# Optimization experiments

Measured on AMD Instinct MI355X. Metric: run time of the kernel, lower is better.

Reference implementation:

```python
import jax, jax.numpy as jnp
import numpy as np

T, N = 12, 1000          # frames, pedestrians
RNN, EMB, GS, OUT = 128, 64, 4, 5
G = GS * GS              # 16 grid cells


def lstm_cell(x, h, c, W_ih, W_hh, b_ih, b_hh):
    # PyTorch LSTMCell gate order: i, f, g, o
    gates = x @ W_ih.T + h @ W_hh.T + b_ih + b_hh
    i, f, g, o = jnp.split(gates, 4, axis=-1)
    c_new = jax.nn.sigmoid(f) * c + jax.nn.sigmoid(i) * jnp.tanh(g)
    h_new = jax.nn.sigmoid(o) * jnp.tanh(c_new)
    return h_new, c_new


def setup_inputs() -> dict:
    key = jax.random.key(0)
    ks = jax.random.split(key, 10)
    s = 0.02  # small init scale for weights
    # binary occupancy grid masks: grid[f, n, p, g] = 1 if ped p falls in cell g of ped n's neighborhood
    grids = (jax.random.uniform(ks[1], (T, N, N, G)) < 0.02).astype(jnp.float32)
    return {
        "input_data": jax.random.normal(ks[0], (T, N, 2), dtype=jnp.float32),
        "grids": grids,
        "hidden_states": jnp.zeros((N, RNN), dtype=jnp.float32),
        "cell_states": jnp.zeros((N, RNN), dtype=jnp.float32),
        "W_in": jax.random.normal(ks[2], (EMB, 2)) * s,
        "b_in": jnp.zeros((EMB,), dtype=jnp.float32),
        "W_soc": jax.random.normal(ks[3], (EMB, G * RNN)) * s,
        "b_soc": jnp.zeros((EMB,), dtype=jnp.float32),
        "W_ih": jax.random.normal(ks[4], (4 * RNN, 2 * EMB)) * s,
        "W_hh": jax.random.normal(ks[5], (4 * RNN, RNN)) * s,
        "b_ih": jnp.zeros((4 * RNN,), dtype=jnp.float32),
        "b_hh": jnp.zeros((4 * RNN,), dtype=jnp.float32),
        "W_out": jax.random.normal(ks[6], (OUT, RNN)) * s,
        "b_out": jnp.zeros((OUT,), dtype=jnp.float32),
    }


def reference(input_data, grids, hidden_states, cell_states,
              W_in, b_in, W_soc, b_soc, W_ih, W_hh, b_ih, b_hh, W_out, b_out):
    def step(carry, frame):
        h, c = carry
        x, grid = frame  # x: [N,2], grid: [N,N,G]
        # social pooling: for each node n, grid[n].T @ h  -> [G, RNN]
        social = jnp.einsum('npg,ph->ngh', grid, h).reshape(N, G * RNN)
        ie = jax.nn.relu(x @ W_in.T + b_in)           # [N, EMB]
        te = jax.nn.relu(social @ W_soc.T + b_soc)    # [N, EMB]
        emb = jnp.concatenate([ie, te], axis=-1)      # [N, 2*EMB]
        h, c = lstm_cell(emb, h, c, W_ih, W_hh, b_ih, b_hh)
        out = h @ W_out.T + b_out                     # [N, OUT]
        return (h, c), out

    (h, c), outputs = jax.lax.scan(step, (hidden_states, cell_states),
                                   (input_data, grids))
    return outputs, h, c  # outputs: [T, N, OUT]
```

## Files before the change

kernel.cpp:

```cpp
#include <hip/hip_runtime.h>
#include <hip/hip_bf16.h>


#define TT   12
#define NN   1000
#define RNNW 128
#define EMBW 64
#define GGW  16
#define OUTD 5
#define UCW  (GGW*EMBW)
#define AKW  256
#define NGATE 512
#define GROW (NN*GGW)

__device__ __forceinline__ float sigmf(float x) { return 1.f / (1.f + __expf(-x)); }

__global__ void k_prep(const float* __restrict__ h0, const float* __restrict__ c0,
                       const float* __restrict__ W_soc,
                       const float* __restrict__ W_ih, const float* __restrict__ W_hh,
                       float* __restrict__ h, float* __restrict__ c,
                       float* __restrict__ WsT, float* __restrict__ WcT) {
    int i = blockIdx.x * 256 + threadIdx.x;
    if (i < 131072) {
        int e = i >> 11, gk = i & 2047;
        WsT[gk * 64 + e] = W_soc[i];
    } else if (i < 196608) {
        int i2 = i - 131072;
        int j = i2 >> 7, k = i2 & 127;
        WcT[k * 512 + j] = W_ih[i2];
    } else if (i < 262144) {
        int i3 = i - 196608;
        int j = i3 >> 7, k = i3 & 127;
        WcT[(128 + k) * 512 + j] = W_hh[i3];
    } else if (i < 262144 + NN * RNNW) {
        int i4 = i - 262144; h[i4] = h0[i4];
    } else if (i < 262144 + 2 * NN * RNNW) {
        int i5 = i - 262144 - NN * RNNW; c[i5] = c0[i5];
    }
}

__global__ __launch_bounds__(256) void k_U(const float* __restrict__ h,
                                           const float* __restrict__ WsT,
                                           float* __restrict__ U) {
    __shared__ float sAT[RNNW][64];
    __shared__ float sBT[RNNW][64];
    const int tid = threadIdx.x;
    const int p0 = blockIdx.x * 64;
    const int g  = blockIdx.y;
    {
        int pp = tid >> 2, kq = (tid & 3) * 4;
        int p = p0 + pp;
        #pragma unroll
        for (int pass = 0; pass < 8; ++pass) {
            int k0 = pass * 16 + kq;
            float4 v = {0.f, 0.f, 0.f, 0.f};
            if (p < NN) v = *(const float4*)(h + (size_t)p * RNNW + k0);
            sAT[k0 + 0][pp] = v.x; sAT[k0 + 1][pp] = v.y;
            sAT[k0 + 2][pp] = v.z; sAT[k0 + 3][pp] = v.w;
        }
    }
    {
        #pragma unroll
        for (int pass = 0; pass < 8; ++pass) {
            int f = pass * 256 + tid;
            int k = f >> 4, e4 = (f & 15) * 4;
            float4 v = *(const float4*)(WsT + (size_t)(g * 128 + k) * 64 + e4);
            *(float4*)(&sBT[k][e4]) = v;
        }
    }
    __syncthreads();
    const int tx = tid & 15, ty = tid >> 4;
    float acc[4][4];
    #pragma unroll
    for (int i = 0; i < 4; i++)
        #pragma unroll
        for (int j = 0; j < 4; j++) acc[i][j] = 0.f;
    #pragma unroll 4
    for (int k = 0; k < RNNW; ++k) {
        float4 a4 = *(const float4*)(&sAT[k][ty * 4]);
        float4 b4 = *(const float4*)(&sBT[k][tx * 4]);
        const float av[4] = {a4.x, a4.y, a4.z, a4.w};
        const float bv[4] = {b4.x, b4.y, b4.z, b4.w};
        #pragma unroll
        for (int i = 0; i < 4; i++)
            #pragma unroll
            for (int j = 0; j < 4; j++) acc[i][j] += av[i] * bv[j];
    }
    #pragma unroll
    for (int i = 0; i < 4; i++) {
        int p = p0 + ty * 4 + i;
        if (p < NN) {
            float4 v = {acc[i][0], acc[i][1], acc[i][2], acc[i][3]};
            *(float4*)(U + (size_t)p * UCW + g * EMBW + tx * 4) = v;
        }
    }
}

__global__ __launch_bounds__(512) void k_pool(const unsigned int* __restrict__ grids,
                                              const float* __restrict__ x_in,
                                              const float* __restrict__ U,
                                              const float* __restrict__ h,
                                              const float* __restrict__ W_in,
                                              const float* __restrict__ b_in,
                                              const float* __restrict__ b_soc,
                                              float* __restrict__ A, int t) {
    const int n = blockIdx.x;
    const int tid = threadIdx.x;
    const int lane = tid & 63, wave = tid >> 6;
    const unsigned int* gp = grids + ((size_t)t * NN + n) * (size_t)GROW;
    float acc = 0.f;
    for (int it = 0; it < 8; ++it) {
        int base = (it * 8 + wave) * 256;
        if (base >= GROW) break;
        int f0 = base + lane * 4;
        uint4 v = {0u, 0u, 0u, 0u};
        if (f0 < GROW) v = *(const uint4*)(gp + f0);
        unsigned int va[4] = {v.x, v.y, v.z, v.w};
        #pragma unroll
        for (int sub = 0; sub < 4; ++sub) {
            unsigned long long m = __ballot(va[sub] != 0u);
            while (m) {
                int b = __builtin_ctzll(m); m &= m - 1;
                int f = base + b * 4 + sub;
                int p = f >> 4, g = f & 15;
                acc += U[(size_t)p * UCW + g * EMBW + lane];
            }
        }
    }
    __shared__ float sAcc[8][64];
    sAcc[wave][lane] = acc;
    __syncthreads();
    if (tid < 64) {
        float s = 0.f;
        #pragma unroll
        for (int w = 0; w < 8; w++) s += sAcc[w][tid];
        float te = fmaxf(s + b_soc[tid], 0.f);
        float x0 = x_in[((size_t)t * NN + n) * 2 + 0];
        float x1 = x_in[((size_t)t * NN + n) * 2 + 1];
        float ie = fmaxf(W_in[tid * 2 + 0] * x0 + W_in[tid * 2 + 1] * x1 + b_in[tid], 0.f);
        A[(size_t)n * AKW + tid] = ie;
        A[(size_t)n * AKW + EMBW + tid] = te;
    } else if (tid >= 128 && tid < 256) {
        int k = tid - 128;
        A[(size_t)n * AKW + 128 + k] = h[(size_t)n * RNNW + k];
    }
}

__global__ __launch_bounds__(256) void k_gates(const float* __restrict__ A,
                                               const float* __restrict__ WcT,
                                               const float* __restrict__ b_ih,
                                               const float* __restrict__ b_hh,
                                               float* __restrict__ gates) {
    __shared__ float sAT[128][32];
    __shared__ float sBT[128][64];
    const int tid = threadIdx.x;
    const int n0 = blockIdx.x * 32;
    const int j0 = blockIdx.y * 64;
    const int tx = tid & 15, ty = tid >> 4;
    float acc[2][4];
    #pragma unroll
    for (int i = 0; i < 2; i++)
        #pragma unroll
        for (int j = 0; j < 4; j++) acc[i][j] = 0.f;
    for (int kc = 0; kc < 2; ++kc) {
        __syncthreads();
        {
            int nn = tid >> 3, kq = (tid & 7) * 4;
            int n = n0 + nn;
            #pragma unroll
            for (int pass = 0; pass < 4; ++pass) {
                int k0 = pass * 32 + kq;
                float4 v = {0.f, 0.f, 0.f, 0.f};
                if (n < NN) v = *(const float4*)(A + (size_t)n * AKW + kc * 128 + k0);
                sAT[k0 + 0][nn] = v.x; sAT[k0 + 1][nn] = v.y;
                sAT[k0 + 2][nn] = v.z; sAT[k0 + 3][nn] = v.w;
            }
        }
        {
            #pragma unroll
            for (int pass = 0; pass < 8; ++pass) {
                int f = pass * 256 + tid;
                int k = f >> 4, e4 = (f & 15) * 4;
                float4 v = *(const float4*)(WcT + (size_t)(kc * 128 + k) * NGATE + j0 + e4);
                *(float4*)(&sBT[k][e4]) = v;
            }
        }
        __syncthreads();
        #pragma unroll 4
        for (int k = 0; k < 128; ++k) {
            float2 a2 = *(const float2*)(&sAT[k][ty * 2]);
            float4 b4 = *(const float4*)(&sBT[k][tx * 4]);
            const float av[2] = {a2.x, a2.y};
            const float bv[4] = {b4.x, b4.y, b4.z, b4.w};
            #pragma unroll
            for (int i = 0; i < 2; i++)
                #pragma unroll
                for (int j = 0; j < 4; j++) acc[i][j] += av[i] * bv[j];
        }
    }
    float4 bi = *(const float4*)(b_ih + j0 + tx * 4);
    float4 bh = *(const float4*)(b_hh + j0 + tx * 4);
    float bias[4] = {bi.x + bh.x, bi.y + bh.y, bi.z + bh.z, bi.w + bh.w};
    #pragma unroll
    for (int i = 0; i < 2; i++) {
        int n = n0 + ty * 2 + i;
        if (n < NN) {
            float4 v = {acc[i][0] + bias[0], acc[i][1] + bias[1],
                        acc[i][2] + bias[2], acc[i][3] + bias[3]};
            *(float4*)(gates + (size_t)n * NGATE + j0 + tx * 4) = v;
        }
    }
}

__global__ __launch_bounds__(256) void k_lstm(const float* __restrict__ gates,
                                              float* __restrict__ h, float* __restrict__ c,
                                              const float* __restrict__ W_out,
                                              const float* __restrict__ b_out,
                                              float* __restrict__ out, int t) {
    __shared__ float sh[2][128];
    int tid = threadIdx.x;
    int local = tid >> 7;
    int r = tid & 127;
    int n = blockIdx.x * 2 + local;
    float hn = 0.f;
    if (n < NN) {
        const float* gr = gates + (size_t)n * NGATE;
        float gi = gr[r], gf = gr[128 + r], gg = gr[256 + r], go = gr[384 + r];
        float cn = sigmf(gf) * c[(size_t)n * RNNW + r] + sigmf(gi) * tanhf(gg);
        hn = sigmf(go) * tanhf(cn);
        c[(size_t)n * RNNW + r] = cn;
        h[(size_t)n * RNNW + r] = hn;
    }
    sh[local][r] = hn;
    __syncthreads();
    if (n < NN && r < OUTD) {
        float s = b_out[r];
        const float* wr = W_out + r * RNNW;
        for (int k = 0; k < RNNW; k++) s += sh[local][k] * wr[k];
        out[((size_t)t * NN + n) * OUTD + r] = s;
    }
}

__global__ void k_final(const float* __restrict__ h, const float* __restrict__ c,
                        float* __restrict__ out) {
    int i = blockIdx.x * 256 + threadIdx.x;
    if (i < NN * RNNW) {
        out[TT * NN * OUTD + i] = h[i];
        out[TT * NN * OUTD + NN * RNNW + i] = c[i];
    }
}

extern "C" void kernel_launch(void* const* d_in, const int* in_sizes, int n_in,
                              void* d_out, int out_size, void* d_ws, size_t ws_size,
                              hipStream_t stream) {
    const float* x_in        = (const float*)d_in[0];
    const unsigned int* grd  = (const unsigned int*)d_in[1];
    const float* h0          = (const float*)d_in[2];
    const float* c0          = (const float*)d_in[3];
    const float* W_in        = (const float*)d_in[4];
    const float* b_in        = (const float*)d_in[5];
    const float* W_soc       = (const float*)d_in[6];
    const float* b_soc       = (const float*)d_in[7];
    const float* W_ih        = (const float*)d_in[8];
    const float* W_hh        = (const float*)d_in[9];
    const float* b_ih        = (const float*)d_in[10];
    const float* b_hh        = (const float*)d_in[11];
    const float* W_out       = (const float*)d_in[12];
    const float* b_out       = (const float*)d_in[13];
    float* out = (float*)d_out;

    float* h     = (float*)d_ws;
    float* c     = h + NN * RNNW;
    float* U     = c + NN * RNNW;
    float* A     = U + (size_t)NN * UCW;
    float* gates = A + (size_t)NN * AKW;
    float* WsT   = gates + (size_t)NN * NGATE;
    float* WcT   = WsT + 2048 * 64;

    hipLaunchKernelGGL(k_prep, dim3(2024), dim3(256), 0, stream,
                       h0, c0, W_soc, W_ih, W_hh, h, c, WsT, WcT);
    for (int t = 0; t < TT; ++t) {
        hipLaunchKernelGGL(k_U,     dim3(16, 16), dim3(256), 0, stream, h, WsT, U);
        hipLaunchKernelGGL(k_pool,  dim3(NN),     dim3(512), 0, stream, grd, x_in, U, h, W_in, b_in, b_soc, A, t);
        hipLaunchKernelGGL(k_gates, dim3(32, 8),  dim3(256), 0, stream, A, WcT, b_ih, b_hh, gates);
        hipLaunchKernelGGL(k_lstm,  dim3(500),    dim3(256), 0, stream, gates, h, c, W_out, b_out, out, t);
    }
    hipLaunchKernelGGL(k_final, dim3(500), dim3(256), 0, stream, h, c, out);
}
```

Measured before the change: 664.2 us.

## Precompute sparse grid indices once and fuse pooling, gate GEMM and LSTM

A new up-front kernel scans all occupancy grids once and stores per-wave lists of nonzero cell indices plus counts, falling back to a dense scan when a list overflows its capacity. The per-step pooling, gate matmul and LSTM/output kernels are merged into one kernel that handles four pedestrians per block. The aim is to cut launches and intermediate gate and activation buffers, and to let the per-step pooling walk compact index lists instead of re-scanning dense grid rows. The cost is an extra index buffer in global memory. The per-block gate matmul also re-reads the full combined weight matrix for every group of four nodes, giving much heavier weight traffic than the previous tiled GEMM.

```diff
diff --git a/kernel.cpp b/kernel.cpp
--- a/kernel.cpp
+++ b/kernel.cpp
@@ -9,9 +9,8 @@
 #define GGW  16
 #define OUTD 5
 #define UCW  (GGW*EMBW)
-#define AKW  256
-#define NGATE 512
 #define GROW (NN*GGW)
+#define RCAP 256
 
 __device__ __forceinline__ float sigmf(float x) { return 1.f / (1.f + __expf(-x)); }
 
@@ -39,6 +38,36 @@
     }
 }
 
+__global__ __launch_bounds__(512) void k_csr(const unsigned int* __restrict__ grids,
+                                             unsigned short* __restrict__ idx,
+                                             unsigned short* __restrict__ cnt) {
+    const int row = blockIdx.x;
+    const int lane = threadIdx.x & 63, wave = threadIdx.x >> 6;
+    const unsigned int* gp = grids + (size_t)row * GROW;
+    unsigned short* wIdx = idx + (size_t)row * (8 * RCAP) + wave * RCAP;
+    int wcnt = 0;
+    for (int it = 0; it < 8; ++it) {
+        int base = (it * 8 + wave) * 256;
+        if (base >= GROW) break;
+        int f0 = base + lane * 4;
+        uint4 v = {0u, 0u, 0u, 0u};
+        if (f0 < GROW) v = *(const uint4*)(gp + f0);
+        unsigned int va[4] = {v.x, v.y, v.z, v.w};
+        #pragma unroll
+        for (int sub = 0; sub < 4; ++sub) {
+            bool nz = (va[sub] != 0u);
+            unsigned long long m = __ballot(nz);
+            if (nz) {
+                int r = __popcll(m & ((1ull << lane) - 1ull));
+                int slot = wcnt + r;
+                if (slot < RCAP) wIdx[slot] = (unsigned short)(f0 + sub);
+            }
+            wcnt += __popcll(m);
+        }
+    }
+    if (lane == 0) cnt[row * 8 + wave] = (unsigned short)(wcnt > RCAP ? 0xFFFF : wcnt);
+}
+
 __global__ __launch_bounds__(256) void k_U(const float* __restrict__ h,
                                            const float* __restrict__ WsT,
                                            float* __restrict__ U) {
@@ -96,147 +125,133 @@
     }
 }
 
-__global__ __launch_bounds__(512) void k_pool(const unsigned int* __restrict__ grids,
-                                              const float* __restrict__ x_in,
-                                              const float* __restrict__ U,
-                                              const float* __restrict__ h,
-                                              const float* __restrict__ W_in,
-                                              const float* __restrict__ b_in,
-                                              const float* __restrict__ b_soc,
-                                              float* __restrict__ A, int t) {
-    const int n = blockIdx.x;
+__global__ __launch_bounds__(512) void k_fused(const unsigned int* __restrict__ grids,
+                                               const unsigned short* __restrict__ idx,
+                                               const unsigned short* __restrict__ cnt,
+                                               const float* __restrict__ x_in,
+                                               const float* __restrict__ U,
+                                               const float* __restrict__ WcT,
+                                               const float* __restrict__ W_in,
+                                               const float* __restrict__ b_in,
+                                               const float* __restrict__ b_soc,
+                                               const float* __restrict__ b_ih,
+                                               const float* __restrict__ b_hh,
+                                               const float* __restrict__ W_out,
+                                               const float* __restrict__ b_out,
+                                               float* __restrict__ A,
+                                               float* __restrict__ h,
+                                               float* __restrict__ c,
+                                               float* __restrict__ out, int t) {
+    __shared__ float sAcc[8][64];
+    __shared__ float sG[4][512];
+    __shared__ float shv[4][128];
     const int tid = threadIdx.x;
     const int lane = tid & 63, wave = tid >> 6;
-    const unsigned int* gp = grids + ((size_t)t * NN + n) * (size_t)GROW;
-    float acc = 0.f;
-    for (int it = 0; it < 8; ++it) {
-        int base = (it * 8 + wave) * 256;
-        if (base >= GROW) break;
-        int f0 = base + lane * 4;
-        uint4 v = {0u, 0u, 0u, 0u};
-        if (f0 < GROW) v = *(const uint4*)(gp + f0);
-        unsigned int va[4] = {v.x, v.y, v.z, v.w};
-        #pragma unroll
-        for (int sub = 0; sub < 4; ++sub) {
-            unsigned long long m = __ballot(va[sub] != 0u);
-            while (m) {
-                int b = __builtin_ctzll(m); m &= m - 1;
-                int f = base + b * 4 + sub;
-                int p = f >> 4, g = f & 15;
-                acc += U[(size_t)p * UCW + g * EMBW + lane];
+    const int n0 = blockIdx.x * 4;
+
+    {
+        const int nl = wave >> 1, half = wave & 1;
+        const int row = t * NN + (n0 + nl);
+        float acc = 0.f;
+        bool fallback = false;
+        #pragma unroll
+        for (int q = 0; q < 4; ++q)
+            if (cnt[row * 8 + half * 4 + q] == 0xFFFF) fallback = true;
+        if (!fallback) {
+            #pragma unroll
+            for (int q = 0; q < 4; ++q) {
+                const int cw = cnt[row * 8 + half * 4 + q];
+                const unsigned short* ip = idx + (size_t)row * (8 * RCAP) + (half * 4 + q) * RCAP;
+                int i = 0;
+                for (; i + 4 <= cw; i += 4) {
+                    int f0 = ip[i], f1 = ip[i + 1], f2 = ip[i + 2], f3 = ip[i + 3];
+                    float u0 = U[((f0 >> 4) << 10) + ((f0 & 15) << 6) + lane];
+                    float u1 = U[((f1 >> 4) << 10) + ((f1 & 15) << 6) + lane];
+                    float u2 = U[((f2 >> 4) << 10) + ((f2 & 15) << 6) + lane];
+                    float u3 = U[((f3 >> 4) << 10) + ((f3 & 15) << 6) + lane];
+                    acc += u0; acc += u1; acc += u2; acc += u3;
+                }
+                for (; i < cw; ++i) {
+                    int f = ip[i];
+                    acc += U[((f >> 4) << 10) + ((f & 15) << 6) + lane];
+                }
             }
-        }
-    }
-    __shared__ float sAcc[8][64];
-    sAcc[wave][lane] = acc;
-    __syncthreads();
-    if (tid < 64) {
-        float s = 0.f;
-        #pragma unroll
-        for (int w = 0; w < 8; w++) s += sAcc[w][tid];
-        float te = fmaxf(s + b_soc[tid], 0.f);
+        } else {
+            const unsigned int* gp = grids + (size_t)row * GROW;
+            #pragma unroll
+            for (int q = 0; q < 4; ++q) {
+                int wv = half * 4 + q;
+                for (int it = 0; it < 8; ++it) {
+                    int base = (it * 8 + wv) * 256;
+                    if (base >= GROW) continue;
+                    int f0 = base + lane * 4;
+                    uint4 v = {0u, 0u, 0u, 0u};
+                    if (f0 < GROW) v = *(const uint4*)(gp + f0);
+                    unsigned int va[4] = {v.x, v.y, v.z, v.w};
+                    #pragma unroll
+                    for (int sub = 0; sub < 4; ++sub) {
+                        unsigned long long m = __ballot(va[sub] != 0u);
+                        while (m) {
+                            int b = __builtin_ctzll(m); m &= m - 1;
+                            int f = base + b * 4 + sub;
+                            acc += U[((f >> 4) << 10) + ((f & 15) << 6) + lane];
+                        }
+                    }
+                }
+            }
+        }
+        sAcc[wave][lane] = acc;
+    }
+    __syncthreads();
+    if (tid < 256) {
+        int nl = tid >> 6, e = tid & 63;
+        int n = n0 + nl;
+        float te = fmaxf(sAcc[2 * nl][e] + sAcc[2 * nl + 1][e] + b_soc[e], 0.f);
         float x0 = x_in[((size_t)t * NN + n) * 2 + 0];
         float x1 = x_in[((size_t)t * NN + n) * 2 + 1];
-        float ie = fmaxf(W_in[tid * 2 + 0] * x0 + W_in[tid * 2 + 1] * x1 + b_in[tid], 0.f);
-        A[(size_t)n * AKW + tid] = ie;
-        A[(size_t)n * AKW + EMBW + tid] = te;
-    } else if (tid >= 128 && tid < 256) {
-        int k = tid - 128;
-        A[(size_t)n * AKW + 128 + k] = h[(size_t)n * RNNW + k];
-    }
-}
-
-__global__ __launch_bounds__(256) void k_gates(const float* __restrict__ A,
-                                               const float* __restrict__ WcT,
-                                               const float* __restrict__ b_ih,
-                                               const float* __restrict__ b_hh,
-                                               float* __restrict__ gates) {
-    __shared__ float sAT[128][32];
-    __shared__ float sBT[128][64];
-    const int tid = threadIdx.x;
-    const int n0 = blockIdx.x * 32;
-    const int j0 = blockIdx.y * 64;
-    const int tx = tid & 15, ty = tid >> 4;
-    float acc[2][4];
-    #pragma unroll
-    for (int i = 0; i < 2; i++)
-        #pragma unroll
-        for (int j = 0; j < 4; j++) acc[i][j] = 0.f;
-    for (int kc = 0; kc < 2; ++kc) {
-        __syncthreads();
-        {
-            int nn = tid >> 3, kq = (tid & 7) * 4;
-            int n = n0 + nn;
-            #pragma unroll
-            for (int pass = 0; pass < 4; ++pass) {
-                int k0 = pass * 32 + kq;
-                float4 v = {0.f, 0.f, 0.f, 0.f};
-                if (n < NN) v = *(const float4*)(A + (size_t)n * AKW + kc * 128 + k0);
-                sAT[k0 + 0][nn] = v.x; sAT[k0 + 1][nn] = v.y;
-                sAT[k0 + 2][nn] = v.z; sAT[k0 + 3][nn] = v.w;
-            }
-        }
-        {
-            #pragma unroll
-            for (int pass = 0; pass < 8; ++pass) {
-                int f = pass * 256 + tid;
-                int k = f >> 4, e4 = (f & 15) * 4;
-                float4 v = *(const float4*)(WcT + (size_t)(kc * 128 + k) * NGATE + j0 + e4);
-                *(float4*)(&sBT[k][e4]) = v;
-            }
-        }
-        __syncthreads();
-        #pragma unroll 4
+        float ie = fmaxf(W_in[e * 2 + 0] * x0 + W_in[e * 2 + 1] * x1 + b_in[e], 0.f);
+        A[(size_t)n * 128 + e]      = ie;
+        A[(size_t)n * 128 + 64 + e] = te;
+    }
+    __syncthreads();
+    {
+        const int j = tid;
+        const float* An = A + (size_t)n0 * 128;
+        const float* hn = h + (size_t)n0 * 128;
+        float g0 = 0.f, g1 = 0.f, g2 = 0.f, g3 = 0.f;
+        #pragma unroll 8
         for (int k = 0; k < 128; ++k) {
-            float2 a2 = *(const float2*)(&sAT[k][ty * 2]);
-            float4 b4 = *(const float4*)(&sBT[k][tx * 4]);
-            const float av[2] = {a2.x, a2.y};
-            const float bv[4] = {b4.x, b4.y, b4.z, b4.w};
-            #pragma unroll
-            for (int i = 0; i < 2; i++)
-                #pragma unroll
-                for (int j = 0; j < 4; j++) acc[i][j] += av[i] * bv[j];
-        }
-    }
-    float4 bi = *(const float4*)(b_ih + j0 + tx * 4);
-    float4 bh = *(const float4*)(b_hh + j0 + tx * 4);
-    float bias[4] = {bi.x + bh.x, bi.y + bh.y, bi.z + bh.z, bi.w + bh.w};
-    #pragma unroll
-    for (int i = 0; i < 2; i++) {
-        int n = n0 + ty * 2 + i;
-        if (n < NN) {
-            float4 v = {acc[i][0] + bias[0], acc[i][1] + bias[1],
-                        acc[i][2] + bias[2], acc[i][3] + bias[3]};
-            *(float4*)(gates + (size_t)n * NGATE + j0 + tx * 4) = v;
-        }
-    }
-}
-
-__global__ __launch_bounds__(256) void k_lstm(const float* __restrict__ gates,
-                                              float* __restrict__ h, float* __restrict__ c,
-                                              const float* __restrict__ W_out,
-                                              const float* __restrict__ b_out,
-                                              float* __restrict__ out, int t) {
-    __shared__ float sh[2][128];
-    int tid = threadIdx.x;
-    int local = tid >> 7;
-    int r = tid & 127;
-    int n = blockIdx.x * 2 + local;
-    float hn = 0.f;
-    if (n < NN) {
-        const float* gr = gates + (size_t)n * NGATE;
-        float gi = gr[r], gf = gr[128 + r], gg = gr[256 + r], go = gr[384 + r];
+            float w = WcT[k * 512 + j];
+            g0 += An[0 * 128 + k] * w; g1 += An[1 * 128 + k] * w;
+            g2 += An[2 * 128 + k] * w; g3 += An[3 * 128 + k] * w;
+        }
+        #pragma unroll 8
+        for (int k = 0; k < 128; ++k) {
+            float w = WcT[(128 + k) * 512 + j];
+            g0 += hn[0 * 128 + k] * w; g1 += hn[1 * 128 + k] * w;
+            g2 += hn[2 * 128 + k] * w; g3 += hn[3 * 128 + k] * w;
+        }
+        float bias = b_ih[j] + b_hh[j];
+        sG[0][j] = g0 + bias; sG[1][j] = g1 + bias;
+        sG[2][j] = g2 + bias; sG[3][j] = g3 + bias;
+    }
+    __syncthreads();
+    {
+        int nl = tid >> 7, r = tid & 127;
+        int n = n0 + nl;
+        float gi = sG[nl][r], gf = sG[nl][128 + r], gg = sG[nl][256 + r], go = sG[nl][384 + r];
         float cn = sigmf(gf) * c[(size_t)n * RNNW + r] + sigmf(gi) * tanhf(gg);
-        hn = sigmf(go) * tanhf(cn);
+        float hn = sigmf(go) * tanhf(cn);
         c[(size_t)n * RNNW + r] = cn;
         h[(size_t)n * RNNW + r] = hn;
-    }
-    sh[local][r] = hn;
-    __syncthreads();
-    if (n < NN && r < OUTD) {
+        shv[nl][r] = hn;
+    }
+    __syncthreads();
+    if ((tid & 127) < OUTD) {
+        int nl = tid >> 7, r = tid & 127, n = n0 + nl;
         float s = b_out[r];
         const float* wr = W_out + r * RNNW;
-        for (int k = 0; k < RNNW; k++) s += sh[local][k] * wr[k];
+        for (int k = 0; k < RNNW; ++k) s += shv[nl][k] * wr[k];
         out[((size_t)t * NN + n) * OUTD + r] = s;
     }
 }
@@ -273,17 +288,19 @@
     float* c     = h + NN * RNNW;
     float* U     = c + NN * RNNW;
     float* A     = U + (size_t)NN * UCW;
-    float* gates = A + (size_t)NN * AKW;
-    float* WsT   = gates + (size_t)NN * NGATE;
+    float* WsT   = A + (size_t)NN * 128;
     float* WcT   = WsT + 2048 * 64;
+    unsigned short* cnt = (unsigned short*)(WcT + 256 * 512);
+    unsigned short* idx = cnt + (size_t)TT * NN * 8;
 
     hipLaunchKernelGGL(k_prep, dim3(2024), dim3(256), 0, stream,
                        h0, c0, W_soc, W_ih, W_hh, h, c, WsT, WcT);
+    hipLaunchKernelGGL(k_csr, dim3(TT * NN), dim3(512), 0, stream, grd, idx, cnt);
     for (int t = 0; t < TT; ++t) {
-        hipLaunchKernelGGL(k_U,     dim3(16, 16), dim3(256), 0, stream, h, WsT, U);
-        hipLaunchKernelGGL(k_pool,  dim3(NN),     dim3(512), 0, stream, grd, x_in, U, h, W_in, b_in, b_soc, A, t);
-        hipLaunchKernelGGL(k_gates, dim3(32, 8),  dim3(256), 0, stream, A, WcT, b_ih, b_hh, gates);
-        hipLaunchKernelGGL(k_lstm,  dim3(500),    dim3(256), 0, stream, gates, h, c, W_out, b_out, out, t);
+        hipLaunchKernelGGL(k_U, dim3(16, 16), dim3(256), 0, stream, h, WsT, U);
+        hipLaunchKernelGGL(k_fused, dim3(NN / 4), dim3(512), 0, stream,
+                           grd, idx, cnt, x_in, U, WcT, W_in, b_in, b_soc,
+                           b_ih, b_hh, W_out, b_out, A, h, c, out, t);
     }
     hipLaunchKernelGGL(k_final, dim3(500), dim3(256), 0, stream, h, c, out);
 }
```

New measurement: 811.0 us. 22.1% more time.

## Fuse gate GEMM with LSTM update and move output projection into k_U

Applied to the files above, without the earlier changes.

Interleaves gate columns in WcT so each thread owns the i,f,g,o values for one hidden unit, which lets the gate GEMM apply the LSTM cell update directly and drops the gates buffer and the separate k_lstm kernel. The output projection for step t now runs inside the next k_U launch, which already stages h in shared memory, and a small tail kernel handles the last step. Final h/c are written during the last step instead of by a separate copy kernel, h is double-buffered, and the pooling loop issues up to four independent U gathers per iteration. Together these cut kernel launches and global round trips per step, at the cost of more code paths to keep consistent.

```diff
diff --git a/kernel.cpp b/kernel.cpp
--- a/kernel.cpp
+++ b/kernel.cpp
@@ -1,25 +1,23 @@
 #include <hip/hip_runtime.h>
-#include <hip/hip_bf16.h>
-
-
-#define TT   12
-#define NN   1000
-#define RNNW 128
-#define EMBW 64
-#define GGW  16
-#define OUTD 5
-#define UCW  (GGW*EMBW)
-#define AKW  256
-#define NGATE 512
-#define GROW (NN*GGW)
+
+
+#define TT    12
+#define NN    1000
+#define RNNW  128
+#define OUTD  5
+#define GROW  16000
+#define UCW   1024
+#define NCHK  63
 
 __device__ __forceinline__ float sigmf(float x) { return 1.f / (1.f + __expf(-x)); }
 
 __global__ void k_prep(const float* __restrict__ h0, const float* __restrict__ c0,
                        const float* __restrict__ W_soc,
                        const float* __restrict__ W_ih, const float* __restrict__ W_hh,
+                       const float* __restrict__ b_ih, const float* __restrict__ b_hh,
                        float* __restrict__ h, float* __restrict__ c,
-                       float* __restrict__ WsT, float* __restrict__ WcT) {
+                       float* __restrict__ WsT, float* __restrict__ WcT,
+                       float* __restrict__ bsum) {
     int i = blockIdx.x * 256 + threadIdx.x;
     if (i < 131072) {
         int e = i >> 11, gk = i & 2047;
@@ -27,21 +25,30 @@
     } else if (i < 196608) {
         int i2 = i - 131072;
         int j = i2 >> 7, k = i2 & 127;
-        WcT[k * 512 + j] = W_ih[i2];
+        int j2 = (j & 127) * 4 + (j >> 7);
+        WcT[k * 512 + j2] = W_ih[i2];
     } else if (i < 262144) {
         int i3 = i - 196608;
         int j = i3 >> 7, k = i3 & 127;
-        WcT[(128 + k) * 512 + j] = W_hh[i3];
-    } else if (i < 262144 + NN * RNNW) {
-        int i4 = i - 262144; h[i4] = h0[i4];
-    } else if (i < 262144 + 2 * NN * RNNW) {
-        int i5 = i - 262144 - NN * RNNW; c[i5] = c0[i5];
+        int j2 = (j & 127) * 4 + (j >> 7);
+        WcT[(128 + k) * 512 + j2] = W_hh[i3];
+    } else if (i < 262656) {
+        int j = i - 262144;
+        int j2 = (j & 127) * 4 + (j >> 7);
+        bsum[j2] = b_ih[j] + b_hh[j];
+    } else if (i < 262656 + NN * RNNW) {
+        int i4 = i - 262656; h[i4] = h0[i4];
+    } else if (i < 262656 + 2 * NN * RNNW) {
+        int i5 = i - 262656 - NN * RNNW; c[i5] = c0[i5];
     }
 }
 
 __global__ __launch_bounds__(256) void k_U(const float* __restrict__ h,
                                            const float* __restrict__ WsT,
-                                           float* __restrict__ U) {
+                                           const float* __restrict__ W_out,
+                                           const float* __restrict__ b_out,
+                                           float* __restrict__ U,
+                                           float* __restrict__ out, int t) {
     __shared__ float sAT[RNNW][64];
     __shared__ float sBT[RNNW][64];
     const int tid = threadIdx.x;
@@ -91,44 +98,65 @@
         int p = p0 + ty * 4 + i;
         if (p < NN) {
             float4 v = {acc[i][0], acc[i][1], acc[i][2], acc[i][3]};
-            *(float4*)(U + (size_t)p * UCW + g * EMBW + tx * 4) = v;
-        }
-    }
-}
-
-__global__ __launch_bounds__(512) void k_pool(const unsigned int* __restrict__ grids,
+            *(float4*)(U + (size_t)p * UCW + g * 64 + tx * 4) = v;
+        }
+    }
+    if (t >= 0 && g == 0) {
+        for (int task = tid; task < 64 * OUTD; task += 256) {
+            int pp = task / OUTD, d = task - pp * OUTD;
+            int p = p0 + pp;
+            if (p < NN) {
+                float s = b_out[d];
+                const float* wr = W_out + d * RNNW;
+                for (int k = 0; k < RNNW; ++k) s += sAT[k][pp] * wr[k];
+                out[((size_t)t * NN + p) * OUTD + d] = s;
+            }
+        }
+    }
+}
+
+__global__ __launch_bounds__(512) void k_pool(const unsigned int* __restrict__ grd,
                                               const float* __restrict__ x_in,
                                               const float* __restrict__ U,
-                                              const float* __restrict__ h,
                                               const float* __restrict__ W_in,
                                               const float* __restrict__ b_in,
                                               const float* __restrict__ b_soc,
                                               float* __restrict__ A, int t) {
     const int n = blockIdx.x;
     const int tid = threadIdx.x;
-    const int lane = tid & 63, wave = tid >> 6;
-    const unsigned int* gp = grids + ((size_t)t * NN + n) * (size_t)GROW;
-    float acc = 0.f;
+    const int lane = tid & 63, wv = tid >> 6;
+    const unsigned int* gp = grd + ((size_t)t * NN + n) * (size_t)GROW;
+    float ac0 = 0.f, ac1 = 0.f, ac2 = 0.f, ac3 = 0.f;
     for (int it = 0; it < 8; ++it) {
-        int base = (it * 8 + wave) * 256;
-        if (base >= GROW) break;
-        int f0 = base + lane * 4;
+        int cc = it * 8 + wv;
+        if (cc >= NCHK) break;
+        int f0 = cc * 256 + lane * 4;
         uint4 v = {0u, 0u, 0u, 0u};
         if (f0 < GROW) v = *(const uint4*)(gp + f0);
-        unsigned int va[4] = {v.x, v.y, v.z, v.w};
-        #pragma unroll
-        for (int sub = 0; sub < 4; ++sub) {
-            unsigned long long m = __ballot(va[sub] != 0u);
-            while (m) {
-                int b = __builtin_ctzll(m); m &= m - 1;
-                int f = base + b * 4 + sub;
-                int p = f >> 4, g = f & 15;
-                acc += U[(size_t)p * UCW + g * EMBW + lane];
-            }
+        unsigned long long m0 = __ballot(v.x != 0u);
+        unsigned long long m1 = __ballot(v.y != 0u);
+        unsigned long long m2 = __ballot(v.z != 0u);
+        unsigned long long m3 = __ballot(v.w != 0u);
+        const int base = cc * 256;
+        while (m0 | m1 | m2 | m3) {
+            float u0 = 0.f, u1 = 0.f, u2 = 0.f, u3 = 0.f;
+            if (m0) { int b = __builtin_ctzll(m0); m0 &= m0 - 1;
+                      int f = base + b * 4 + 0;
+                      u0 = U[(size_t)(f >> 4) * UCW + (f & 15) * 64 + lane]; }
+            if (m1) { int b = __builtin_ctzll(m1); m1 &= m1 - 1;
+                      int f = base + b * 4 + 1;
+                      u1 = U[(size_t)(f >> 4) * UCW + (f & 15) * 64 + lane]; }
+            if (m2) { int b = __builtin_ctzll(m2); m2 &= m2 - 1;
+                      int f = base + b * 4 + 2;
+                      u2 = U[(size_t)(f >> 4) * UCW + (f & 15) * 64 + lane]; }
+            if (m3) { int b = __builtin_ctzll(m3); m3 &= m3 - 1;
+                      int f = base + b * 4 + 3;
+                      u3 = U[(size_t)(f >> 4) * UCW + (f & 15) * 64 + lane]; }
+            ac0 += u0; ac1 += u1; ac2 += u2; ac3 += u3;
         }
     }
     __shared__ float sAcc[8][64];
-    sAcc[wave][lane] = acc;
+    sAcc[wv][lane] = (ac0 + ac1) + (ac2 + ac3);
     __syncthreads();
     if (tid < 64) {
         float s = 0.f;
@@ -138,19 +166,18 @@
         float x0 = x_in[((size_t)t * NN + n) * 2 + 0];
         float x1 = x_in[((size_t)t * NN + n) * 2 + 1];
         float ie = fmaxf(W_in[tid * 2 + 0] * x0 + W_in[tid * 2 + 1] * x1 + b_in[tid], 0.f);
-        A[(size_t)n * AKW + tid] = ie;
-        A[(size_t)n * AKW + EMBW + tid] = te;
-    } else if (tid >= 128 && tid < 256) {
-        int k = tid - 128;
-        A[(size_t)n * AKW + 128 + k] = h[(size_t)n * RNNW + k];
-    }
-}
-
-__global__ __launch_bounds__(256) void k_gates(const float* __restrict__ A,
-                                               const float* __restrict__ WcT,
-                                               const float* __restrict__ b_ih,
-                                               const float* __restrict__ b_hh,
-                                               float* __restrict__ gates) {
+        A[(size_t)n * RNNW + tid]      = ie;
+        A[(size_t)n * RNNW + 64 + tid] = te;
+    }
+}
+
+__global__ __launch_bounds__(256) void k_gl(const float* __restrict__ A,
+                                            const float* __restrict__ hin,
+                                            float* __restrict__ hout,
+                                            float* __restrict__ c,
+                                            const float* __restrict__ WcT,
+                                            const float* __restrict__ bsum,
+                                            float* __restrict__ out, int t) {
     __shared__ float sAT[128][32];
     __shared__ float sBT[128][64];
     const int tid = threadIdx.x;
@@ -167,11 +194,12 @@
         {
             int nn = tid >> 3, kq = (tid & 7) * 4;
             int n = n0 + nn;
+            const float* src = kc ? (hin + (size_t)n * RNNW) : (A + (size_t)n * RNNW);
             #pragma unroll
             for (int pass = 0; pass < 4; ++pass) {
                 int k0 = pass * 32 + kq;
                 float4 v = {0.f, 0.f, 0.f, 0.f};
-                if (n < NN) v = *(const float4*)(A + (size_t)n * AKW + kc * 128 + k0);
+                if (n < NN) v = *(const float4*)(src + k0);
                 sAT[k0 + 0][nn] = v.x; sAT[k0 + 1][nn] = v.y;
                 sAT[k0 + 2][nn] = v.z; sAT[k0 + 3][nn] = v.w;
             }
@@ -181,7 +209,7 @@
             for (int pass = 0; pass < 8; ++pass) {
                 int f = pass * 256 + tid;
                 int k = f >> 4, e4 = (f & 15) * 4;
-                float4 v = *(const float4*)(WcT + (size_t)(kc * 128 + k) * NGATE + j0 + e4);
+                float4 v = *(const float4*)(WcT + (size_t)(kc * 128 + k) * 512 + j0 + e4);
                 *(float4*)(&sBT[k][e4]) = v;
             }
         }
@@ -198,92 +226,87 @@
                 for (int j = 0; j < 4; j++) acc[i][j] += av[i] * bv[j];
         }
     }
-    float4 bi = *(const float4*)(b_ih + j0 + tx * 4);
-    float4 bh = *(const float4*)(b_hh + j0 + tx * 4);
-    float bias[4] = {bi.x + bh.x, bi.y + bh.y, bi.z + bh.z, bi.w + bh.w};
+    float4 bs = *(const float4*)(bsum + j0 + tx * 4);
+    const int r = (j0 >> 2) + tx;
     #pragma unroll
     for (int i = 0; i < 2; i++) {
         int n = n0 + ty * 2 + i;
         if (n < NN) {
-            float4 v = {acc[i][0] + bias[0], acc[i][1] + bias[1],
-                        acc[i][2] + bias[2], acc[i][3] + bias[3]};
-            *(float4*)(gates + (size_t)n * NGATE + j0 + tx * 4) = v;
-        }
-    }
-}
-
-__global__ __launch_bounds__(256) void k_lstm(const float* __restrict__ gates,
-                                              float* __restrict__ h, float* __restrict__ c,
+            float gi = acc[i][0] + bs.x;
+            float gf = acc[i][1] + bs.y;
+            float gg = acc[i][2] + bs.z;
+            float go = acc[i][3] + bs.w;
+            float cn = sigmf(gf) * c[(size_t)n * RNNW + r] + sigmf(gi) * tanhf(gg);
+            float hn = sigmf(go) * tanhf(cn);
+            c[(size_t)n * RNNW + r] = cn;
+            hout[(size_t)n * RNNW + r] = hn;
+            if (t == TT - 1) {
+                out[(size_t)TT * NN * OUTD + (size_t)n * RNNW + r] = hn;
+                out[(size_t)TT * NN * OUTD + (size_t)NN * RNNW + (size_t)n * RNNW + r] = cn;
+            }
+        }
+    }
+}
+
+__global__ __launch_bounds__(256) void k_tail(const float* __restrict__ h,
                                               const float* __restrict__ W_out,
                                               const float* __restrict__ b_out,
-                                              float* __restrict__ out, int t) {
-    __shared__ float sh[2][128];
-    int tid = threadIdx.x;
-    int local = tid >> 7;
-    int r = tid & 127;
-    int n = blockIdx.x * 2 + local;
-    float hn = 0.f;
-    if (n < NN) {
-        const float* gr = gates + (size_t)n * NGATE;
-        float gi = gr[r], gf = gr[128 + r], gg = gr[256 + r], go = gr[384 + r];
-        float cn = sigmf(gf) * c[(size_t)n * RNNW + r] + sigmf(gi) * tanhf(gg);
-        hn = sigmf(go) * tanhf(cn);
-        c[(size_t)n * RNNW + r] = cn;
-        h[(size_t)n * RNNW + r] = hn;
-    }
-    sh[local][r] = hn;
-    __syncthreads();
-    if (n < NN && r < OUTD) {
-        float s = b_out[r];
-        const float* wr = W_out + r * RNNW;
-        for (int k = 0; k < RNNW; k++) s += sh[local][k] * wr[k];
-        out[((size_t)t * NN + n) * OUTD + r] = s;
-    }
-}
-
-__global__ void k_final(const float* __restrict__ h, const float* __restrict__ c,
-                        float* __restrict__ out) {
-    int i = blockIdx.x * 256 + threadIdx.x;
-    if (i < NN * RNNW) {
-        out[TT * NN * OUTD + i] = h[i];
-        out[TT * NN * OUTD + NN * RNNW + i] = c[i];
+                                              float* __restrict__ out) {
+    int task = blockIdx.x * 256 + threadIdx.x;
+    if (task < NN * OUTD) {
+        int p = task / OUTD, d = task - p * OUTD;
+        float s = b_out[d];
+        const float* wr = W_out + d * RNNW;
+        const float* hp = h + (size_t)p * RNNW;
+        for (int k = 0; k < RNNW; ++k) s += hp[k] * wr[k];
+        out[((size_t)(TT - 1) * NN + p) * OUTD + d] = s;
     }
 }
 
 extern "C" void kernel_launch(void* const* d_in, const int* in_sizes, int n_in,
                               void* d_out, int out_size, void* d_ws, size_t ws_size,
                               hipStream_t stream) {
-    const float* x_in        = (const float*)d_in[0];
-    const unsigned int* grd  = (const unsigned int*)d_in[1];
-    const float* h0          = (const float*)d_in[2];
-    const float* c0          = (const float*)d_in[3];
-    const float* W_in        = (const float*)d_in[4];
-    const float* b_in        = (const float*)d_in[5];
-    const float* W_soc       = (const float*)d_in[6];
-    const float* b_soc       = (const float*)d_in[7];
-    const float* W_ih        = (const float*)d_in[8];
-    const float* W_hh        = (const float*)d_in[9];
-    const float* b_ih        = (const float*)d_in[10];
-    const float* b_hh        = (const float*)d_in[11];
-    const float* W_out       = (const float*)d_in[12];
-    const float* b_out       = (const float*)d_in[13];
+    const float* x_in       = (const float*)d_in[0];
+    const unsigned int* grd = (const unsigned int*)d_in[1];
+    const float* h0         = (const float*)d_in[2];
+    const float* c0         = (const float*)d_in[3];
+    const float* W_in       = (const float*)d_in[4];
+    const float* b_in       = (const float*)d_in[5];
+    const float* W_soc      = (const float*)d_in[6];
+    const float* b_soc      = (const float*)d_in[7];
+    const float* W_ih       = (const float*)d_in[8];
+    const float* W_hh       = (const float*)d_in[9];
+    const float* b_ih       = (const float*)d_in[10];
+    const float* b_hh       = (const float*)d_in[11];
+    const float* W_out      = (const float*)d_in[12];
+    const float* b_out      = (const float*)d_in[13];
     float* out = (float*)d_out;
 
-    float* h     = (float*)d_ws;
-    float* c     = h + NN * RNNW;
-    float* U     = c + NN * RNNW;
-    float* A     = U + (size_t)NN * UCW;
-    float* gates = A + (size_t)NN * AKW;
-    float* WsT   = gates + (size_t)NN * NGATE;
-    float* WcT   = WsT + 2048 * 64;
-
-    hipLaunchKernelGGL(k_prep, dim3(2024), dim3(256), 0, stream,
-                       h0, c0, W_soc, W_ih, W_hh, h, c, WsT, WcT);
+    float* hb0  = (float*)d_ws;
+    float* hb1  = hb0 + NN * RNNW;
+    float* c    = hb1 + NN * RNNW;
+    float* U    = c + NN * RNNW;
+    float* A    = U + (size_t)NN * UCW;
+    float* WsT  = A + (size_t)NN * RNNW;
+    float* WcT  = WsT + 131072;
+    float* bsum = WcT + 131072;
+
+    hipLaunchKernelGGL(k_prep, dim3(2026), dim3(256), 0, stream,
+                       h0, c0, W_soc, W_ih, W_hh, b_ih, b_hh, hb0, c, WsT, WcT, bsum);
+    hipLaunchKernelGGL(k_U, dim3(16, 16), dim3(256), 0, stream,
+                       hb0, WsT, W_out, b_out, U, out, -1);
     for (int t = 0; t < TT; ++t) {
-        hipLaunchKernelGGL(k_U,     dim3(16, 16), dim3(256), 0, stream, h, WsT, U);
-        hipLaunchKernelGGL(k_pool,  dim3(NN),     dim3(512), 0, stream, grd, x_in, U, h, W_in, b_in, b_soc, A, t);
-        hipLaunchKernelGGL(k_gates, dim3(32, 8),  dim3(256), 0, stream, A, WcT, b_ih, b_hh, gates);
-        hipLaunchKernelGGL(k_lstm,  dim3(500),    dim3(256), 0, stream, gates, h, c, W_out, b_out, out, t);
-    }
-    hipLaunchKernelGGL(k_final, dim3(500), dim3(256), 0, stream, h, c, out);
-}
+        float* hin  = (t & 1) ? hb1 : hb0;
+        float* hout = (t & 1) ? hb0 : hb1;
+        hipLaunchKernelGGL(k_pool, dim3(NN), dim3(512), 0, stream,
+                           grd, x_in, U, W_in, b_in, b_soc, A, t);
+        hipLaunchKernelGGL(k_gl, dim3(32, 8), dim3(256), 0, stream,
+                           A, hin, hout, c, WcT, bsum, out, t);
+        if (t < TT - 1) {
+            hipLaunchKernelGGL(k_U, dim3(16, 16), dim3(256), 0, stream,
+                               hout, WsT, W_out, b_out, U, out, t);
+        }
+    }
+    hipLaunchKernelGGL(k_tail, dim3(20), dim3(256), 0, stream,
+                       hb0, W_out, b_out, out);
+}
```

New measurement: 641.8 us, median of 2. 3.4% less time.
